# Performance work log

Hardware: AMD Instinct MI355X
Metric: run time of the kernel (lower is better)

## Reference

```python
import jax, jax.numpy as jnp
import numpy as np

B = 65536
MOTION, HIDDEN, LATENT, OUT = 256, 256, 64, 256
E, GH = 6, 64
INPUT = LATENT + MOTION   # 320, decoder layer-0 input width
INTER = LATENT + HIDDEN   # 320, decoder layers 1-3 input width


def _elu(x):
    return jax.nn.elu(x)


def _ln(x, s, b):
    m = jnp.mean(x, -1, keepdims=True)
    v = jnp.mean((x - m) ** 2, -1, keepdims=True)
    return (x - m) / jnp.sqrt(v + 1e-5) * s + b


def setup_inputs() -> dict:
    key = jax.random.key(0)
    ks = iter(jax.random.split(key, 64))

    def nrm(shape, scale=0.05):
        return jax.random.normal(next(ks), shape, jnp.float32) * scale

    d1 = [INPUT, INTER, INTER, INTER]   # per-layer expert weight in-dims
    d2 = [HIDDEN, HIDDEN, HIDDEN, OUT]  # per-layer expert weight out-dims
    inp = {
        'curr_state': jax.random.normal(next(ks), (B, MOTION), jnp.float32),
        'next_state': jax.random.normal(next(ks), (B, MOTION), jnp.float32),
        'eps': jax.random.normal(next(ks), (B, LATENT), jnp.float32),
        # encoder (torch Linear stored as [in, out])
        'enc_w1': nrm((2 * MOTION, HIDDEN)), 'enc_b1': nrm((HIDDEN,)),
        'enc_w2': nrm((HIDDEN, HIDDEN)), 'enc_b2': nrm((HIDDEN,)),
        'mu_w': nrm((HIDDEN, LATENT)), 'mu_b': nrm((LATENT,)),
        'lv_w': nrm((HIDDEN, LATENT)), 'lv_b': nrm((LATENT,)),
        # gating MLP
        'g_w1': nrm((INPUT, GH)), 'g_b1': nrm((GH,)),
        'g_w2': nrm((GH, GH)), 'g_b2': nrm((GH,)),
        'g_w3': nrm((GH, E)), 'g_b3': nrm((E,)),
    }
    for i in range(4):
        stdv = 1.0 / np.sqrt(d1[i])
        inp[f'w{i}'] = jax.random.uniform(next(ks), (E, d1[i], d2[i]), jnp.float32, -stdv, stdv)
        inp[f'b{i}'] = jax.random.uniform(next(ks), (E, d2[i]), jnp.float32, -stdv, stdv)
        inp[f'ln{i}_s'] = jnp.ones((d1[i],), jnp.float32)
        inp[f'ln{i}_b'] = jnp.zeros((d1[i],), jnp.float32)
    return inp


def reference(curr_state, next_state, eps,
              enc_w1, enc_b1, enc_w2, enc_b2, mu_w, mu_b, lv_w, lv_b,
              g_w1, g_b1, g_w2, g_b2, g_w3, g_b3,
              w0, b0, ln0_s, ln0_b, w1, b1, ln1_s, ln1_b,
              w2, b2, ln2_s, ln2_b, w3, b3, ln3_s, ln3_b):
    # ---- encoder ----
    h = _elu(jnp.concatenate([curr_state, next_state], -1) @ enc_w1 + enc_b1)
    h = _elu(h @ enc_w2 + enc_b2)
    mu = h @ mu_w + mu_b
    logvar = h @ lv_w + lv_b
    z = mu + eps * jnp.exp(0.5 * logvar)
    # ---- decoder(mu, curr_state): softmax-gated expert-weight blending ----
    x0 = jnp.concatenate([mu, curr_state], -1)            # [B, INPUT]
    g = _elu(x0 @ g_w1 + g_b1)
    g = _elu(g @ g_w2 + g_b2)
    coef = jax.nn.softmax(g @ g_w3 + g_b3, axis=-1)       # [B, E]
    ws, bs = (w0, w1, w2, w3), (b0, b1, b2, b3)
    lns = ((ln0_s, ln0_b), (ln1_s, ln1_b), (ln2_s, ln2_b), (ln3_s, ln3_b))
    out = None
    for i in range(4):
        xin = x0 if i == 0 else jnp.concatenate([mu, out], -1)
        xin = _ln(xin, *lns[i])
        mix = jnp.einsum('be,bj,ejk->bk', coef, xin, ws[i]) + coef @ bs[i]
        if i == 0:
            out = _elu(mix)
        elif i < 3:
            out = _elu(out + mix)
        else:
            out = mix
    return (out, z, mu, logvar)
```

## Files before the change

kernel.cpp:

```cpp
#include <hip/hip_runtime.h>
#include <hip/hip_bf16.h>
#include <stdint.h>


#define NB 65536
#define CHUNK 8192

typedef __attribute__((ext_vector_type(8))) short bf16x8;
typedef __attribute__((ext_vector_type(4))) float f32x4;

union FragU { bf16x8 v; unsigned int w[4]; uint4 u4; };

#define WP_E1   0
#define WP_E2   262144
#define WP_MULV 393216
#define WP_G1   458752
#define WP_G2   499712
#define WP_G3   507904
#define WP_DEC  509952
#define WP_BDEC 4442112
#define WP_COEF 4466688

#define L_XN     0
#define L_SCR    81920
#define L_WB     98304
#define LDS_ENC  147456
#define L_MUF   (L_XN + 2*CHUNK)
#define L_LVF   L_WB
#define L_HG1   L_WB
#define L_HG2   (L_WB + 32768)
#define L_G2W   L_SCR
#define L_G3W   (L_SCR + 8192)
#define L_SCORE (L_SCR + 10240)

#define B_XN     0
#define B_RAWMU  81920
#define B_COEF   98304
#define B_STATS  101376
#define B_PART   102400
#define B_PARTMU 106496
#define B_MUSTAT 110592
#define LDS_DEC  111616

__device__ __forceinline__ unsigned int pack2(float a, float b){
    __hip_bfloat162 h = __float22bfloat162_rn(make_float2(a, b));
    union { __hip_bfloat162 h2; unsigned int u; } cv; cv.h2 = h; return cv.u;
}
__device__ __forceinline__ unsigned short f2bf(float a){
    __hip_bfloat16 h = __float2bfloat16(a);
    union { __hip_bfloat16 h1; unsigned short u; } cv; cv.h1 = h; return cv.u;
}
__device__ __forceinline__ float eluf(float x){ return x > 0.f ? x : expm1f(x); }
__device__ __forceinline__ f32x4 mfma16(bf16x8 a, bf16x8 b, f32x4 c){
    return __builtin_amdgcn_mfma_f32_16x16x32_bf16(a, b, c, 0, 0, 0);
}
__device__ __forceinline__ void gload16(const void* g, void* l){
    __builtin_amdgcn_global_load_lds(
        (__attribute__((address_space(1))) unsigned int*)(uintptr_t)g,
        (__attribute__((address_space(3))) unsigned int*)(unsigned int)(uintptr_t)l,
        16, 0, 0);
}

template<int N> __device__ __forceinline__ void pipeV(){
    __builtin_amdgcn_sched_barrier(0);
    asm volatile("s_waitcnt vmcnt(%0)" :: "n"(N) : "memory");
    asm volatile("s_barrier" ::: "memory");
    __builtin_amdgcn_sched_barrier(0);
}
template<int N> __device__ __forceinline__ void pipeVL(){
    __builtin_amdgcn_sched_barrier(0);
    asm volatile("s_waitcnt vmcnt(%0) lgkmcnt(0)" :: "n"(N) : "memory");
    asm volatile("s_barrier" ::: "memory");
    __builtin_amdgcn_sched_barrier(0);
}
__device__ __forceinline__ void pipeL(){
    __builtin_amdgcn_sched_barrier(0);
    asm volatile("s_waitcnt lgkmcnt(0)" ::: "memory");
    asm volatile("s_barrier" ::: "memory");
    __builtin_amdgcn_sched_barrier(0);
}

__global__ void pack_small(const float* __restrict__ e1w, const float* __restrict__ e2w,
                           const float* __restrict__ muw, const float* __restrict__ lvw,
                           const float* __restrict__ g1w, const float* __restrict__ g2w,
                           const float* __restrict__ g3w, unsigned short* __restrict__ wsh){
    int p = blockIdx.x*256 + threadIdx.x;
    int local, k, n;
    auto decode = [&](int base, int NN){
        local = p - base;
        int i = local & 7, ln = (local>>3)&63, rest = local>>9;
        int ntg = rest % (NN/16), kb = rest / (NN/16);
        k = kb*32 + (ln>>4)*8 + i; n = ntg*16 + (ln&15);
    };
    if (p < 131072)      { decode(0,      256); wsh[WP_E1/2   + local] = f2bf(e1w[k*256+n]); }
    else if (p < 196608) { decode(131072, 256); wsh[WP_E2/2   + local] = f2bf(e2w[k*256+n]); }
    else if (p < 229376) { decode(196608, 128); wsh[WP_MULV/2 + local] = f2bf(n < 64 ? muw[k*64+n] : lvw[k*64+n-64]); }
    else if (p < 249856) { decode(229376,  64); wsh[WP_G1/2   + local] = f2bf(g1w[k*64+n]); }
    else if (p < 253952) { decode(249856,  64); wsh[WP_G2/2   + local] = f2bf(g2w[k*64+n]); }
    else                 { decode(253952,  16); wsh[WP_G3/2   + local] = f2bf(n < 6 ? g3w[k*6+n] : 0.f); }
}

__global__ void pack_dec(const float* __restrict__ w0, const float* __restrict__ w1,
                         const float* __restrict__ w2, const float* __restrict__ w3,
                         const float* __restrict__ s0, const float* __restrict__ s1,
                         const float* __restrict__ s2, const float* __restrict__ s3,
                         unsigned short* __restrict__ wsh){
    int p = blockIdx.x*256 + threadIdx.x;
    int i = p & 7, ln = (p>>3)&63, rest = p>>9;
    int ntg = rest & 15, r2 = rest >> 4;
    int kb = r2 % 10, r3 = r2 / 10;
    int e = r3 % 6, L = r3 / 6;
    int k = kb*32 + (ln>>4)*8 + i;
    int n = ntg*16 + (ln&15);
    const float* w = (L==0)?w0:(L==1)?w1:(L==2)?w2:w3;
    const float* s = (L==0)?s0:(L==1)?s1:(L==2)?s2:s3;
    wsh[WP_DEC/2 + p] = f2bf(s[k] * w[(e*320+k)*256 + n]);
}

__global__ void pack_bdec(const float* __restrict__ w0, const float* __restrict__ w1,
                          const float* __restrict__ w2, const float* __restrict__ w3,
                          const float* __restrict__ b0, const float* __restrict__ b1,
                          const float* __restrict__ b2, const float* __restrict__ b3,
                          const float* __restrict__ t0, const float* __restrict__ t1,
                          const float* __restrict__ t2, const float* __restrict__ t3,
                          float* __restrict__ outp){
    int t = blockIdx.x*256 + threadIdx.x;
    int n = t & 255, r = t >> 8;
    int e = r % 6, L = r / 6;
    const float* w  = (L==0)?w0:(L==1)?w1:(L==2)?w2:w3;
    const float* b  = (L==0)?b0:(L==1)?b1:(L==2)?b2:b3;
    const float* lb = (L==0)?t0:(L==1)?t1:(L==2)?t2:t3;
    float acc = b[e*256 + n];
    for (int k = 0; k < 320; ++k) acc += lb[k] * w[(e*320+k)*256 + n];
    outp[(L*6+e)*256 + n] = acc;
}

__global__ __launch_bounds__(512, 2) void vae_enc(
    const float* __restrict__ curr, const float* __restrict__ nxt,
    const float* __restrict__ eps,
    const float* __restrict__ eb1, const float* __restrict__ eb2,
    const float* __restrict__ mub, const float* __restrict__ lvb,
    const float* __restrict__ gb1, const float* __restrict__ gb2,
    const float* __restrict__ gb3,
    const unsigned short* __restrict__ wsh,
    float* __restrict__ coefws, float* __restrict__ dout)
{
    __shared__ __align__(16) char sm[LDS_ENC];
    const int tid  = threadIdx.x;
    const int lane = tid & 63;
    const int wave = tid >> 6;
    const int wr   = wave >> 2;
    const int wc   = wave & 3;
    const int l15  = lane & 15;
    const int lh   = lane >> 4;
    const long row0 = (long)blockIdx.x * 128;
    const char* wsb = (const char*)wsh;
    const f32x4 Z4 = {0.f, 0.f, 0.f, 0.f};

    const int aswz = ((lh ^ ((l15 >> 1) & 3)) << 4);
    int aoff[4];
    #pragma unroll
    for (int mt = 0; mt < 4; ++mt)
        aoff[mt] = ((((wr << 6) + (mt << 4) + l15)) << 6) + aswz;

    auto WB = [&](int i) -> int { return L_WB + i*16384; };
    auto stage16 = [&](long gOff, int ldsBase){
        gload16(wsb + gOff + ((long)wave << 10) + (lane << 4), sm + ldsBase + (wave << 10));
        gload16(wsb + gOff + ((long)(wave + 8) << 10) + (lane << 4), sm + ldsBase + ((wave + 8) << 10));
    };
    auto stage8 = [&](long gOff, int ldsBase){
        gload16(wsb + gOff + ((long)wave << 10) + (lane << 4), sm + ldsBase + (wave << 10));
    };
    auto stage4 = [&](long gOff, int ldsBase){
        int u = wave & 3;
        gload16(wsb + gOff + ((long)u << 10) + (lane << 4), sm + ldsBase + (u << 10));
    };
    auto loadB = [&](int bufBase, int idx) -> bf16x8 {
        FragU f; f.u4 = *(const uint4*)(sm + bufBase + (idx << 10) + (lane << 4));
        return f.v;
    };
    auto putRow = [&](int base, int n, int mt, const f32x4& v){
        char* cb = sm + base + ((n >> 5) * CHUNK);
        int col = n & 31;
        #pragma unroll
        for (int j = 0; j < 4; ++j){
            int r = (wr << 6) + (mt << 4) + (lh << 2) + j;
            *(unsigned short*)(cb + (r << 6) + ((((col >> 3) ^ ((r >> 1) & 3))) << 4)
                               + ((col & 7) << 1)) = f2bf(v[j]);
        }
    };

    f32x4 acc4[4][4];
    #pragma unroll
    for (int a = 0; a < 4; ++a)
        #pragma unroll
        for (int b = 0; b < 4; ++b) acc4[a][b] = Z4;
    {
        const int xrow = tid >> 2, xg = tid & 3;
        float4 xa, xb;
        auto loadX = [&](int kb){
            const float* src = (kb < 8) ? curr : nxt;
            const float* p = src + (row0 + xrow)*256 + (kb & 7)*32 + xg*8;
            xa = *(const float4*)p; xb = *(const float4*)(p + 4);
        };
        auto packX = [&](int slot){
            uint4 pk;
            pk.x = pack2(xa.x, xa.y); pk.y = pack2(xa.z, xa.w);
            pk.z = pack2(xb.x, xb.y); pk.w = pack2(xb.z, xb.w);
            *(uint4*)(sm + L_XN + slot*CHUNK + (xrow << 6)
                      + ((xg ^ ((xrow >> 1) & 3)) << 4)) = pk;
        };
        stage16(WP_E1, WB(0)); stage16(WP_E1 + 16384, WB(1));
        loadX(0); packX(0);
        loadX(1);
        #pragma unroll 1
        for (int s = 0; s < 16; ++s){
            pipeVL<4>();
            if (s + 2 < 16) stage16(WP_E1 + (long)(s + 2)*16384, WB((s + 2) % 3));
            if (s + 1 < 16){
                packX((s + 1) & 1);
                if (s + 2 < 16) loadX(s + 2);
            }
            int xbuf = L_XN + (s & 1)*CHUNK;
            int wb = WB(s % 3);
            FragU a[4];
            #pragma unroll
            for (int mt = 0; mt < 4; ++mt) a[mt].u4 = *(const uint4*)(sm + xbuf + aoff[mt]);
            #pragma unroll
            for (int nt = 0; nt < 4; ++nt){
                bf16x8 b = loadB(wb, wc*4 + nt);
                #pragma unroll
                for (int mt = 0; mt < 4; ++mt) acc4[mt][nt] = mfma16(a[mt].v, b, acc4[mt][nt]);
            }
        }
        pipeL();
        #pragma unroll
        for (int nt = 0; nt < 4; ++nt){
            int n = wc*64 + nt*16 + l15;
            float bias = eb1[n];
            #pragma unroll
            for (int mt = 0; mt < 4; ++mt){
                f32x4 v;
                #pragma unroll
                for (int j = 0; j < 4; ++j) v[j] = eluf(acc4[mt][nt][j] + bias);
                putRow(L_XN, n, mt, v);
            }
        }
        stage16(WP_E2, WB(0)); stage16(WP_E2 + 16384, WB(1));
        pipeL();
    }
    #pragma unroll
    for (int a = 0; a < 4; ++a)
        #pragma unroll
        for (int b = 0; b < 4; ++b) acc4[a][b] = Z4;
    {
        #pragma unroll 1
        for (int s = 0; s < 8; ++s){
            if (s + 1 < 8) pipeV<2>(); else pipeV<0>();
            if (s + 2 < 8) stage16(WP_E2 + (long)(s + 2)*16384, WB((s + 2) % 3));
            int wb = WB(s % 3);
            FragU a[4];
            #pragma unroll
            for (int mt = 0; mt < 4; ++mt)
                a[mt].u4 = *(const uint4*)(sm + L_XN + s*CHUNK + aoff[mt]);
            #pragma unroll
            for (int nt = 0; nt < 4; ++nt){
                bf16x8 b = loadB(wb, wc*4 + nt);
                #pragma unroll
                for (int mt = 0; mt < 4; ++mt) acc4[mt][nt] = mfma16(a[mt].v, b, acc4[mt][nt]);
            }
        }
        pipeL();
        #pragma unroll
        for (int nt = 0; nt < 4; ++nt){
            int n = wc*64 + nt*16 + l15;
            float bias = eb2[n];
            #pragma unroll
            for (int mt = 0; mt < 4; ++mt){
                f32x4 v;
                #pragma unroll
                for (int j = 0; j < 4; ++j) v[j] = eluf(acc4[mt][nt][j] + bias);
                putRow(L_XN, n, mt, v);
            }
        }
        stage8(WP_MULV, WB(0)); stage8(WP_MULV + 8192, WB(1));
        pipeL();
    }
    {
        f32x4 am[4][2];
        #pragma unroll
        for (int a = 0; a < 4; ++a){ am[a][0] = Z4; am[a][1] = Z4; }
        #pragma unroll 1
        for (int s = 0; s < 8; ++s){
            if (s + 1 < 8) pipeV<1>(); else pipeV<0>();
            if (s + 2 < 8) stage8(WP_MULV + (long)(s + 2)*8192, WB((s + 2) % 3));
            int wb = WB(s % 3);
            FragU a[4];
            #pragma unroll
            for (int mt = 0; mt < 4; ++mt)
                a[mt].u4 = *(const uint4*)(sm + L_XN + s*CHUNK + aoff[mt]);
            #pragma unroll
            for (int nt = 0; nt < 2; ++nt){
                bf16x8 b = loadB(wb, wc*2 + nt);
                #pragma unroll
                for (int mt = 0; mt < 4; ++mt) am[mt][nt] = mfma16(a[mt].v, b, am[mt][nt]);
            }
        }
        pipeL();
        #pragma unroll
        for (int nt = 0; nt < 2; ++nt){
            int n = wc*32 + nt*16 + l15;
            if (n < 64){
                float bias = mub[n];
                #pragma unroll
                for (int mt = 0; mt < 4; ++mt)
                    #pragma unroll
                    for (int j = 0; j < 4; ++j){
                        int r = (wr << 6) + (mt << 4) + (lh << 2) + j;
                        float v = am[mt][nt][j] + bias;
                        *(float*)(sm + L_MUF + (r << 8) + (n << 2)) = v;
                        dout[(long)NB*320 + (row0 + r)*64 + n] = v;
                    }
            } else {
                float bias = lvb[n - 64];
                #pragma unroll
                for (int mt = 0; mt < 4; ++mt)
                    #pragma unroll
                    for (int j = 0; j < 4; ++j){
                        int r = (wr << 6) + (mt << 4) + (lh << 2) + j;
                        float v = am[mt][nt][j] + bias;
                        *(float*)(sm + L_LVF + (r << 8) + ((n - 64) << 2)) = v;
                        dout[(long)NB*384 + (row0 + r)*64 + (n - 64)] = v;
                    }
            }
        }
        pipeL();
    }
    {
        int row = tid >> 2, seg = (tid & 3) << 4;
        float zm[16], zl[16];
        #pragma unroll
        for (int q = 0; q < 4; ++q){
            float4 m4 = *(const float4*)(sm + L_MUF + (row << 8) + ((seg + q*4) << 2));
            float4 l4 = *(const float4*)(sm + L_LVF + (row << 8) + ((seg + q*4) << 2));
            zm[q*4+0]=m4.x; zm[q*4+1]=m4.y; zm[q*4+2]=m4.z; zm[q*4+3]=m4.w;
            zl[q*4+0]=l4.x; zl[q*4+1]=l4.y; zl[q*4+2]=l4.z; zl[q*4+3]=l4.w;
        }
        const float* ep = eps + (row0 + row)*64 + seg;
        float* zo = dout + (long)NB*256 + (row0 + row)*64 + seg;
        #pragma unroll
        for (int q = 0; q < 4; ++q){
            float4 e4 = *(const float4*)(ep + q*4);
            float4 z4;
            z4.x = zm[q*4+0] + e4.x * expf(0.5f*zl[q*4+0]);
            z4.y = zm[q*4+1] + e4.y * expf(0.5f*zl[q*4+1]);
            z4.z = zm[q*4+2] + e4.z * expf(0.5f*zl[q*4+2]);
            z4.w = zm[q*4+3] + e4.w * expf(0.5f*zl[q*4+3]);
            *(float4*)(zo + q*4) = z4;
        }
        uint4 pkA, pkB;
        pkA.x = pack2(zm[0],  zm[1]);  pkA.y = pack2(zm[2],  zm[3]);
        pkA.z = pack2(zm[4],  zm[5]);  pkA.w = pack2(zm[6],  zm[7]);
        pkB.x = pack2(zm[8],  zm[9]);  pkB.y = pack2(zm[10], zm[11]);
        pkB.z = pack2(zm[12], zm[13]); pkB.w = pack2(zm[14], zm[15]);
        int c = seg >> 5, g0 = (seg & 31) >> 3, sw = (row >> 1) & 3;
        char* cb = sm + L_XN + c*CHUNK + (row << 6);
        *(uint4*)(cb + ((g0 ^ sw) << 4))       = pkA;
        *(uint4*)(cb + (((g0 + 1) ^ sw) << 4)) = pkB;
    }
    pipeL();
    #pragma unroll
    for (int c = 0; c < 2; ++c){
        int idx = c*512 + tid;
        int row = idx & 127, kbi = idx >> 7;
        const float* p = curr + (row0 + row)*256 + kbi*32;
        char* cb = sm + L_XN + (2 + kbi)*CHUNK + (row << 6);
        int sw = (row >> 1) & 3;
        #pragma unroll
        for (int g = 0; g < 4; ++g){
            float4 fa = *(const float4*)(p + g*8);
            float4 fb = *(const float4*)(p + g*8 + 4);
            uint4 pk;
            pk.x = pack2(fa.x, fa.y); pk.y = pack2(fa.z, fa.w);
            pk.z = pack2(fb.x, fb.y); pk.w = pack2(fb.z, fb.w);
            *(uint4*)(cb + ((g ^ sw) << 4)) = pk;
        }
    }
    stage4(WP_G1, WB(0)); stage4(WP_G1 + 4096, WB(1));
    pipeL();
    {
        f32x4 ga[4];
        #pragma unroll
        for (int a = 0; a < 4; ++a) ga[a] = Z4;
        #pragma unroll 1
        for (int s = 0; s < 10; ++s){
            if (s + 1 < 10) pipeV<1>(); else pipeV<0>();
            if (s + 2 < 10) stage4(WP_G1 + (long)(s + 2)*4096, WB((s + 2) % 3));
            int wb = WB(s % 3);
            bf16x8 b = loadB(wb, wc);
            #pragma unroll
            for (int mt = 0; mt < 4; ++mt){
                FragU a; a.u4 = *(const uint4*)(sm + L_XN + s*CHUNK + aoff[mt]);
                ga[mt] = mfma16(a.v, b, ga[mt]);
            }
        }
        pipeL();
        {
            int n = wc*16 + l15;
            float bias = gb1[n];
            #pragma unroll
            for (int mt = 0; mt < 4; ++mt){
                f32x4 v;
                #pragma unroll
                for (int j = 0; j < 4; ++j) v[j] = eluf(ga[mt][j] + bias);
                putRow(L_HG1, n, mt, v);
            }
        }
        stage8(WP_G2, L_G2W);
        if (wave < 2)
            gload16(wsb + WP_G3 + ((long)wave << 10) + (lane << 4),
                    sm + L_G3W + (wave << 10));
        pipeVL<0>();
        #pragma unroll
        for (int a = 0; a < 4; ++a) ga[a] = Z4;
        #pragma unroll
        for (int kb = 0; kb < 2; ++kb){
            bf16x8 b = loadB(L_G2W, kb*4 + wc);
            #pragma unroll
            for (int mt = 0; mt < 4; ++mt){
                FragU a; a.u4 = *(const uint4*)(sm + L_HG1 + kb*CHUNK + aoff[mt]);
                ga[mt] = mfma16(a.v, b, ga[mt]);
            }
        }
        pipeL();
        {
            int n = wc*16 + l15;
            float bias = gb2[n];
            #pragma unroll
            for (int mt = 0; mt < 4; ++mt){
                f32x4 v;
                #pragma unroll
                for (int j = 0; j < 4; ++j) v[j] = eluf(ga[mt][j] + bias);
                putRow(L_HG2, n, mt, v);
            }
        }
        pipeL();
        if (wc == 0){
            f32x4 sc[4];
            #pragma unroll
            for (int a = 0; a < 4; ++a) sc[a] = Z4;
            #pragma unroll
            for (int kb = 0; kb < 2; ++kb){
                bf16x8 b = loadB(L_G3W, kb);
                #pragma unroll
                for (int mt = 0; mt < 4; ++mt){
                    FragU a; a.u4 = *(const uint4*)(sm + L_HG2 + kb*CHUNK + aoff[mt]);
                    sc[mt] = mfma16(a.v, b, sc[mt]);
                }
            }
            if (l15 < 8){
                float bias = (l15 < 6) ? gb3[l15] : 0.f;
                #pragma unroll
                for (int mt = 0; mt < 4; ++mt)
                    #pragma unroll
                    for (int j = 0; j < 4; ++j){
                        int r = (wr << 6) + (mt << 4) + (lh << 2) + j;
                        *(float*)(sm + L_SCORE + (r << 5) + (l15 << 2)) = sc[mt][j] + bias;
                    }
            }
        }
        pipeL();
        if (tid < 128){
            float s[6];
            #pragma unroll
            for (int e = 0; e < 6; ++e) s[e] = *(const float*)(sm + L_SCORE + (tid << 5) + (e << 2));
            float m = s[0];
            #pragma unroll
            for (int e = 1; e < 6; ++e) m = fmaxf(m, s[e]);
            float sum = 0.f;
            #pragma unroll
            for (int e = 0; e < 6; ++e){ s[e] = expf(s[e] - m); sum += s[e]; }
            float inv = 1.f / sum;
            float* cw = coefws + (long)blockIdx.x * 768;
            #pragma unroll
            for (int e = 0; e < 6; ++e) cw[e*128 + tid] = s[e] * inv;
        }
    }
}

__global__ __launch_bounds__(512, 2) void vae_dec(
    const float* __restrict__ curr,
    const unsigned short* __restrict__ wsh, const float* __restrict__ bdec,
    const float* __restrict__ coefws, float* __restrict__ dout)
{
    __shared__ __align__(16) char sm[LDS_DEC];
    const int tid  = threadIdx.x;
    const int lane = tid & 63;
    const int wave = tid >> 6;
    const int wr   = wave >> 2;
    const int wc   = wave & 3;
    const int l15  = lane & 15;
    const int lh   = lane >> 4;
    const long row0 = (long)blockIdx.x * 128;
    const char* wsb = (const char*)wsh;
    const f32x4 Z4 = {0.f, 0.f, 0.f, 0.f};

    const int aswz = ((lh ^ ((l15 >> 1) & 3)) << 4);
    int aoff[4];
    #pragma unroll
    for (int mt = 0; mt < 4; ++mt)
        aoff[mt] = ((((wr << 6) + (mt << 4) + l15)) << 6) + aswz;

    auto putRow = [&](int base, int n, int mt, const f32x4& v){
        char* cb = sm + base + ((n >> 5) * CHUNK);
        int col = n & 31;
        #pragma unroll
        for (int j = 0; j < 4; ++j){
            int r = (wr << 6) + (mt << 4) + (lh << 2) + j;
            *(unsigned short*)(cb + (r << 6) + ((((col >> 3) ^ ((r >> 1) & 3))) << 4)
                               + ((col & 7) << 1)) = f2bf(v[j]);
        }
    };

    #pragma unroll
    for (int rep = 0; rep < 2; ++rep){
        int i = rep*512 + tid;
        if (i < 768) *(float*)(sm + B_COEF + (i << 2)) = coefws[(long)blockIdx.x*768 + i];
    }
    {
        int row = tid >> 2, seg = (tid & 3) << 4;
        const float* mp = dout + (long)NB*320 + (row0 + row)*64 + seg;
        float zm[16];
        #pragma unroll
        for (int q = 0; q < 4; ++q){
            float4 m4 = *(const float4*)(mp + q*4);
            zm[q*4+0]=m4.x; zm[q*4+1]=m4.y; zm[q*4+2]=m4.z; zm[q*4+3]=m4.w;
        }
        uint4 pkA, pkB;
        pkA.x = pack2(zm[0],  zm[1]);  pkA.y = pack2(zm[2],  zm[3]);
        pkA.z = pack2(zm[4],  zm[5]);  pkA.w = pack2(zm[6],  zm[7]);
        pkB.x = pack2(zm[8],  zm[9]);  pkB.y = pack2(zm[10], zm[11]);
        pkB.z = pack2(zm[12], zm[13]); pkB.w = pack2(zm[14], zm[15]);
        int c = seg >> 5, g0 = (seg & 31) >> 3, sw = (row >> 1) & 3;
        char* cb = sm + B_XN + c*CHUNK + (row << 6);
        *(uint4*)(cb + ((g0 ^ sw) << 4))       = pkA;
        *(uint4*)(cb + (((g0 + 1) ^ sw) << 4)) = pkB;
    }
    #pragma unroll
    for (int c = 0; c < 2; ++c){
        int idx = c*512 + tid;
        int row = idx & 127, kbi = idx >> 7;
        const float* p = curr + (row0 + row)*256 + kbi*32;
        char* cb = sm + B_XN + (2 + kbi)*CHUNK + (row << 6);
        int sw = (row >> 1) & 3;
        #pragma unroll
        for (int g = 0; g < 4; ++g){
            float4 fa = *(const float4*)(p + g*8);
            float4 fb = *(const float4*)(p + g*8 + 4);
            uint4 pk;
            pk.x = pack2(fa.x, fa.y); pk.y = pack2(fa.z, fa.w);
            pk.z = pack2(fb.x, fb.y); pk.w = pack2(fb.z, fb.w);
            *(uint4*)(cb + ((g ^ sw) << 4)) = pk;
        }
    }
    __syncthreads();
    {
        int row = tid >> 2, part = tid & 3;
        int go = ((part ^ ((row >> 1) & 3)) << 4);
        float s = 0.f, q = 0.f, smu = 0.f, qmu = 0.f;
        #pragma unroll
        for (int c = 0; c < 10; ++c){
            uint4 d = *(const uint4*)(sm + B_XN + c*CHUNK + (row << 6) + go);
            const unsigned int* dw = (const unsigned int*)&d;
            float ls = 0.f, lq = 0.f;
            #pragma unroll
            for (int u = 0; u < 4; ++u){
                float lo = __uint_as_float(dw[u] << 16);
                float hi = __uint_as_float(dw[u] & 0xffff0000u);
                ls += lo + hi; lq += lo*lo + hi*hi;
            }
            s += ls; q += lq;
            if (c < 2){ smu += ls; qmu += lq; }
        }
        *(float2*)(sm + B_PART   + (((row << 2) + part) << 3)) = make_float2(s, q);
        *(float2*)(sm + B_PARTMU + (((row << 2) + part) << 3)) = make_float2(smu, qmu);
    }
    __syncthreads();
    if (tid < 128){
        float S = 0.f, Q = 0.f, Sm = 0.f, Qm = 0.f;
        #pragma unroll
        for (int pp = 0; pp < 4; ++pp){
            float2 f = *(const float2*)(sm + B_PART   + (((tid << 2) + pp) << 3));
            float2 g = *(const float2*)(sm + B_PARTMU + (((tid << 2) + pp) << 3));
            S += f.x; Q += f.y; Sm += g.x; Qm += g.y;
        }
        float mean = S * (1.f/320.f);
        float var  = Q * (1.f/320.f) - mean*mean;
        *(float2*)(sm + B_STATS  + (tid << 3)) = make_float2(mean, rsqrtf(var + 1e-5f));
        *(float2*)(sm + B_MUSTAT + (tid << 3)) = make_float2(Sm, Qm);
    }
    __syncthreads();
    {
        int row = tid >> 2, part = tid & 3;
        int go = ((part ^ ((row >> 1) & 3)) << 4);
        float2 st = *(const float2*)(sm + B_STATS + (row << 3));
        #pragma unroll
        for (int c = 0; c < 10; ++c){
            char* p = sm + B_XN + c*CHUNK + (row << 6) + go;
            uint4 d = *(const uint4*)p;
            if (c < 2) *(uint4*)(sm + B_RAWMU + c*CHUNK + (row << 6) + go) = d;
            const unsigned int* dw = (const unsigned int*)&d;
            uint4 o; unsigned int* ow = (unsigned int*)&o;
            #pragma unroll
            for (int u = 0; u < 4; ++u){
                float lo = (__uint_as_float(dw[u] << 16)         - st.x) * st.y;
                float hi = (__uint_as_float(dw[u] & 0xffff0000u) - st.x) * st.y;
                ow[u] = pack2(lo, hi);
            }
            *(uint4*)p = o;
        }
    }
    __syncthreads();

    f32x4 master[4][4], acc[4][4];
    #pragma unroll
    for (int a = 0; a < 4; ++a)
        #pragma unroll
        for (int b = 0; b < 4; ++b) master[a][b] = Z4;

    #pragma unroll 1
    for (int L = 0; L < 4; ++L){
        const char* wLb = wsb + WP_DEC + (((long)L*60) << 14) + (lane << 4)
                          + ((wc*4) << 10);
        FragU bA[4], bB[4];
        auto loadBG = [&](FragU* bd, int s){
            const char* p = wLb + ((long)s << 14);
            #pragma unroll
            for (int nt = 0; nt < 4; ++nt)
                bd[nt].u4 = *(const uint4*)(p + (nt << 10));
        };
        auto doStep = [&](FragU* bd, int s){
            int e  = s / 10;
            int kb = s - e*10;
            FragU a[4];
            #pragma unroll
            for (int mt = 0; mt < 4; ++mt)
                a[mt].u4 = *(const uint4*)(sm + B_XN + kb*CHUNK + aoff[mt]);
            if (kb == 0){
                #pragma unroll
                for (int x = 0; x < 4; ++x)
                    #pragma unroll
                    for (int y = 0; y < 4; ++y) acc[x][y] = Z4;
            }
            #pragma unroll
            for (int nt = 0; nt < 4; ++nt)
                #pragma unroll
                for (int mt = 0; mt < 4; ++mt)
                    acc[mt][nt] = mfma16(a[mt].v, bd[nt].v, acc[mt][nt]);
            if (kb == 9){
                #pragma unroll
                for (int mt = 0; mt < 4; ++mt){
                    f32x4 cq = *(const f32x4*)(sm + B_COEF +
                                ((e*128 + (wr << 6) + (mt << 4) + (lh << 2)) << 2));
                    #pragma unroll
                    for (int nt = 0; nt < 4; ++nt)
                        #pragma unroll
                        for (int j = 0; j < 4; ++j)
                            master[mt][nt][j] = fmaf(cq[j], acc[mt][nt][j], master[mt][nt][j]);
                }
            }
        };
        loadBG(bA, 0);
        #pragma unroll 1
        for (int s = 0; s < 60; s += 2){
            loadBG(bB, s + 1);
            doStep(bA, s);
            if (s + 2 < 60) loadBG(bA, s + 2);
            doStep(bB, s + 1);
        }
        __syncthreads();

        {
            float bv[6][4];
            #pragma unroll
            for (int ee = 0; ee < 6; ++ee)
                #pragma unroll
                for (int nt = 0; nt < 4; ++nt)
                    bv[ee][nt] = bdec[((L*6 + ee) << 8) + wc*64 + nt*16 + l15];
            #pragma unroll
            for (int mt = 0; mt < 4; ++mt){
                f32x4 cq[6];
                #pragma unroll
                for (int ee = 0; ee < 6; ++ee)
                    cq[ee] = *(const f32x4*)(sm + B_COEF +
                              ((ee*128 + (wr << 6) + (mt << 4) + (lh << 2)) << 2));
                #pragma unroll
                for (int nt = 0; nt < 4; ++nt){
                    int n = wc*64 + nt*16 + l15;
                    f32x4 v;
                    #pragma unroll
                    for (int j = 0; j < 4; ++j){
                        float bias = cq[0][j]*bv[0][nt] + cq[1][j]*bv[1][nt]
                                   + cq[2][j]*bv[2][nt] + cq[3][j]*bv[3][nt]
                                   + cq[4][j]*bv[4][nt] + cq[5][j]*bv[5][nt];
                        float mix = master[mt][nt][j] + bias;
                        v[j] = (L == 3) ? mix : eluf(mix);
                    }
                    if (L < 3){
                        acc[mt][nt] = v;
                        master[mt][nt] = (L < 2) ? v : Z4;
                    } else {
                        #pragma unroll
                        for (int j = 0; j < 4; ++j){
                            int r = (wr << 6) + (mt << 4) + (lh << 2) + j;
                            dout[(row0 + r)*256 + n] = v[j];
                        }
                    }
                }
            }
        }
        if (L < 3){
            #pragma unroll
            for (int mt = 0; mt < 4; ++mt){
                f32x4 sv = acc[mt][0] + acc[mt][1] + acc[mt][2] + acc[mt][3];
                f32x4 qv = acc[mt][0]*acc[mt][0] + acc[mt][1]*acc[mt][1]
                         + acc[mt][2]*acc[mt][2] + acc[mt][3]*acc[mt][3];
                #pragma unroll
                for (int x = 1; x < 16; x <<= 1){
                    #pragma unroll
                    for (int j = 0; j < 4; ++j){
                        sv[j] += __shfl_xor(sv[j], x);
                        qv[j] += __shfl_xor(qv[j], x);
                    }
                }
                if (l15 == 0){
                    #pragma unroll
                    for (int j = 0; j < 4; ++j){
                        int r = (wr << 6) + (mt << 4) + (lh << 2) + j;
                        *(float2*)(sm + B_PART + (((r << 2) + wc) << 3)) = make_float2(sv[j], qv[j]);
                    }
                }
            }
            __syncthreads();
            if (tid < 128){
                float2 mu2 = *(const float2*)(sm + B_MUSTAT + (tid << 3));
                float S = mu2.x, Q = mu2.y;
                #pragma unroll
                for (int pp = 0; pp < 4; ++pp){
                    float2 f = *(const float2*)(sm + B_PART + (((tid << 2) + pp) << 3));
                    S += f.x; Q += f.y;
                }
                float mean = S * (1.f/320.f);
                float var  = Q * (1.f/320.f) - mean*mean;
                *(float2*)(sm + B_STATS + (tid << 3)) = make_float2(mean, rsqrtf(var + 1e-5f));
            }
            __syncthreads();
            #pragma unroll
            for (int mt = 0; mt < 4; ++mt){
                int r0 = (wr << 6) + (mt << 4) + (lh << 2);
                float4 p0 = *(const float4*)(sm + B_STATS + (r0 << 3));
                float4 p1 = *(const float4*)(sm + B_STATS + (r0 << 3) + 16);
                float mj[4] = {p0.x, p0.z, p1.x, p1.z};
                float rj[4] = {p0.y, p0.w, p1.y, p1.w};
                #pragma unroll
                for (int nt = 0; nt < 4; ++nt){
                    int n = wc*64 + nt*16 + l15;
                    f32x4 xn;
                    #pragma unroll
                    for (int j = 0; j < 4; ++j) xn[j] = (acc[mt][nt][j] - mj[j]) * rj[j];
                    putRow(B_XN + 2*CHUNK, n, mt, xn);
                }
            }
            #pragma unroll
            for (int rep = 0; rep < 2; ++rep){
                int gi = rep*512 + tid;
                int c = gi >> 9, row = (gi >> 2) & 127, g2 = gi & 3;
                float2 st = *(const float2*)(sm + B_STATS + (row << 3));
                uint4 d = *(const uint4*)(sm + B_RAWMU + c*CHUNK + (row << 6) + (g2 << 4));
                const unsigned int* dw = (const unsigned int*)&d;
                uint4 o; unsigned int* ow = (unsigned int*)&o;
                #pragma unroll
                for (int u = 0; u < 4; ++u){
                    float lo = (__uint_as_float(dw[u] << 16)         - st.x) * st.y;
                    float hi = (__uint_as_float(dw[u] & 0xffff0000u) - st.x) * st.y;
                    ow[u] = pack2(lo, hi);
                }
                *(uint4*)(sm + B_XN + c*CHUNK + (row << 6) + (g2 << 4)) = o;
            }
            __syncthreads();
        }
    }
}

extern "C" void kernel_launch(void* const* d_in, const int* in_sizes, int n_in,
                              void* d_out, int out_size, void* d_ws, size_t ws_size,
                              hipStream_t stream)
{
    (void)in_sizes; (void)n_in; (void)out_size; (void)ws_size;
    const float* curr = (const float*)d_in[0];
    const float* nxt  = (const float*)d_in[1];
    const float* eps  = (const float*)d_in[2];
    const float* ew1  = (const float*)d_in[3];
    const float* eb1  = (const float*)d_in[4];
    const float* ew2  = (const float*)d_in[5];
    const float* eb2  = (const float*)d_in[6];
    const float* muw  = (const float*)d_in[7];
    const float* mub  = (const float*)d_in[8];
    const float* lvw  = (const float*)d_in[9];
    const float* lvb  = (const float*)d_in[10];
    const float* gw1  = (const float*)d_in[11];
    const float* gb1  = (const float*)d_in[12];
    const float* gw2  = (const float*)d_in[13];
    const float* gb2  = (const float*)d_in[14];
    const float* gw3  = (const float*)d_in[15];
    const float* gb3  = (const float*)d_in[16];
    const float* w0 = (const float*)d_in[17]; const float* b0 = (const float*)d_in[18];
    const float* s0 = (const float*)d_in[19]; const float* t0 = (const float*)d_in[20];
    const float* w1 = (const float*)d_in[21]; const float* b1 = (const float*)d_in[22];
    const float* s1 = (const float*)d_in[23]; const float* t1 = (const float*)d_in[24];
    const float* w2 = (const float*)d_in[25]; const float* b2 = (const float*)d_in[26];
    const float* s2 = (const float*)d_in[27]; const float* t2 = (const float*)d_in[28];
    const float* w3 = (const float*)d_in[29]; const float* b3 = (const float*)d_in[30];
    const float* s3 = (const float*)d_in[31]; const float* t3 = (const float*)d_in[32];

    unsigned short* wsh = (unsigned short*)d_ws;
    float* bdec   = (float*)((char*)d_ws + WP_BDEC);
    float* coefws = (float*)((char*)d_ws + WP_COEF);
    float* dout   = (float*)d_out;

    hipLaunchKernelGGL(pack_small, dim3(996), dim3(256), 0, stream,
                       ew1, ew2, muw, lvw, gw1, gw2, gw3, wsh);
    hipLaunchKernelGGL(pack_dec, dim3(7680), dim3(256), 0, stream,
                       w0, w1, w2, w3, s0, s1, s2, s3, wsh);
    hipLaunchKernelGGL(pack_bdec, dim3(24), dim3(256), 0, stream,
                       w0, w1, w2, w3, b0, b1, b2, b3, t0, t1, t2, t3, bdec);
    hipLaunchKernelGGL(vae_enc, dim3(512), dim3(512), 0, stream,
                       curr, nxt, eps, eb1, eb2, mub, lvb, gb1, gb2, gb3,
                       wsh, coefws, dout);
    hipLaunchKernelGGL(vae_dec, dim3(512), dim3(512), 0, stream,
                       curr, wsh, bdec, coefws, dout);
}
```

Measured before the change: 530.6 us.

## Halve decoder block rows to 64 for higher occupancy and smaller LDS

The decoder kernel now processes 64 rows per block instead of 128. All 8 waves share those rows and each wave takes a 32-column slice of the output. The raw-mu LDS copy is dropped and mu is re-read from global memory at each layer, which shrinks LDS to about 51KB and allows launch bounds of 4 blocks per CU with twice as many blocks. In exchange, each block reads the same B weight fragments for half as many rows, doubling weight traffic from L2, and there are extra global reloads of mu.

Result: faster. 496.5 us (-6.4%).

```diff
diff --git a/kernel.cpp b/kernel.cpp
--- a/kernel.cpp
+++ b/kernel.cpp
@@ -5,6 +5,7 @@
 
 #define NB 65536
 #define CHUNK 8192
+#define CH64  4096
 
 typedef __attribute__((ext_vector_type(8))) short bf16x8;
 typedef __attribute__((ext_vector_type(4))) float f32x4;
@@ -33,14 +34,13 @@
 #define L_G3W   (L_SCR + 8192)
 #define L_SCORE (L_SCR + 10240)
 
-#define B_XN     0
-#define B_RAWMU  81920
-#define B_COEF   98304
-#define B_STATS  101376
-#define B_PART   102400
-#define B_PARTMU 106496
-#define B_MUSTAT 110592
-#define LDS_DEC  111616
+#define D_XN     0
+#define D_COEF   40960
+#define D_STATS  42496
+#define D_PART   43008
+#define D_PARTMU 47104
+#define D_MUSTAT 51200
+#define LDS_DEC  51712
 
 __device__ __forceinline__ unsigned int pack2(float a, float b){
     __hip_bfloat162 h = __float22bfloat162_rn(make_float2(a, b));
@@ -488,7 +488,7 @@
     }
 }
 
-__global__ __launch_bounds__(512, 2) void vae_dec(
+__global__ __launch_bounds__(512, 4) void vae_dec(
     const float* __restrict__ curr,
     const unsigned short* __restrict__ wsh, const float* __restrict__ bdec,
     const float* __restrict__ coefws, float* __restrict__ dout)
@@ -496,12 +496,11 @@
     __shared__ __align__(16) char sm[LDS_DEC];
     const int tid  = threadIdx.x;
     const int lane = tid & 63;
-    const int wave = tid >> 6;
-    const int wr   = wave >> 2;
-    const int wc   = wave & 3;
+    const int w    = tid >> 6;
     const int l15  = lane & 15;
     const int lh   = lane >> 4;
-    const long row0 = (long)blockIdx.x * 128;
+    const long row0 = (long)blockIdx.x * 64;
+    const int eb   = blockIdx.x >> 1, half = blockIdx.x & 1;
     const char* wsb = (const char*)wsh;
     const f32x4 Z4 = {0.f, 0.f, 0.f, 0.f};
 
@@ -509,49 +508,37 @@
     int aoff[4];
     #pragma unroll
     for (int mt = 0; mt < 4; ++mt)
-        aoff[mt] = ((((wr << 6) + (mt << 4) + l15)) << 6) + aswz;
+        aoff[mt] = (((mt << 4) + l15) << 6) + aswz;
 
     auto putRow = [&](int base, int n, int mt, const f32x4& v){
-        char* cb = sm + base + ((n >> 5) * CHUNK);
+        char* cb = sm + base + ((n >> 5) * CH64);
         int col = n & 31;
         #pragma unroll
         for (int j = 0; j < 4; ++j){
-            int r = (wr << 6) + (mt << 4) + (lh << 2) + j;
+            int r = (mt << 4) + (lh << 2) + j;
             *(unsigned short*)(cb + (r << 6) + ((((col >> 3) ^ ((r >> 1) & 3))) << 4)
                                + ((col & 7) << 1)) = f2bf(v[j]);
         }
     };
 
-    #pragma unroll
-    for (int rep = 0; rep < 2; ++rep){
-        int i = rep*512 + tid;
-        if (i < 768) *(float*)(sm + B_COEF + (i << 2)) = coefws[(long)blockIdx.x*768 + i];
-    }
+    if (tid < 384)
+        *(float*)(sm + D_COEF + (tid << 2)) =
+            coefws[(long)eb*768 + (tid >> 6)*128 + half*64 + (tid & 63)];
     {
-        int row = tid >> 2, seg = (tid & 3) << 4;
+        int row = tid >> 3, seg = (tid & 7) << 3;
         const float* mp = dout + (long)NB*320 + (row0 + row)*64 + seg;
-        float zm[16];
-        #pragma unroll
-        for (int q = 0; q < 4; ++q){
-            float4 m4 = *(const float4*)(mp + q*4);
-            zm[q*4+0]=m4.x; zm[q*4+1]=m4.y; zm[q*4+2]=m4.z; zm[q*4+3]=m4.w;
-        }
-        uint4 pkA, pkB;
-        pkA.x = pack2(zm[0],  zm[1]);  pkA.y = pack2(zm[2],  zm[3]);
-        pkA.z = pack2(zm[4],  zm[5]);  pkA.w = pack2(zm[6],  zm[7]);
-        pkB.x = pack2(zm[8],  zm[9]);  pkB.y = pack2(zm[10], zm[11]);
-        pkB.z = pack2(zm[12], zm[13]); pkB.w = pack2(zm[14], zm[15]);
-        int c = seg >> 5, g0 = (seg & 31) >> 3, sw = (row >> 1) & 3;
-        char* cb = sm + B_XN + c*CHUNK + (row << 6);
-        *(uint4*)(cb + ((g0 ^ sw) << 4))       = pkA;
-        *(uint4*)(cb + (((g0 + 1) ^ sw) << 4)) = pkB;
-    }
-    #pragma unroll
-    for (int c = 0; c < 2; ++c){
-        int idx = c*512 + tid;
-        int row = idx & 127, kbi = idx >> 7;
+        float4 a4 = *(const float4*)mp;
+        float4 b4 = *(const float4*)(mp + 4);
+        uint4 pk;
+        pk.x = pack2(a4.x, a4.y); pk.y = pack2(a4.z, a4.w);
+        pk.z = pack2(b4.x, b4.y); pk.w = pack2(b4.z, b4.w);
+        int g0 = seg >> 3, c = g0 >> 2, gg = g0 & 3, sw = (row >> 1) & 3;
+        *(uint4*)(sm + D_XN + c*CH64 + (row << 6) + ((gg ^ sw) << 4)) = pk;
+    }
+    {
+        int row = tid & 63, kbi = tid >> 6;
         const float* p = curr + (row0 + row)*256 + kbi*32;
-        char* cb = sm + B_XN + (2 + kbi)*CHUNK + (row << 6);
+        char* cb = sm + D_XN + (2 + kbi)*CH64 + (row << 6);
         int sw = (row >> 1) & 3;
         #pragma unroll
         for (int g = 0; g < 4; ++g){
@@ -565,12 +552,14 @@
     }
     __syncthreads();
     {
-        int row = tid >> 2, part = tid & 3;
-        int go = ((part ^ ((row >> 1) & 3)) << 4);
+        int row = tid >> 3, part = tid & 7;
+        int sw = (row >> 1) & 3;
         float s = 0.f, q = 0.f, smu = 0.f, qmu = 0.f;
         #pragma unroll
-        for (int c = 0; c < 10; ++c){
-            uint4 d = *(const uint4*)(sm + B_XN + c*CHUNK + (row << 6) + go);
+        for (int k = 0; k < 5; ++k){
+            int g = part + (k << 3);
+            int c = g >> 2, gg = g & 3;
+            uint4 d = *(const uint4*)(sm + D_XN + c*CH64 + (row << 6) + ((gg ^ sw) << 4));
             const unsigned int* dw = (const unsigned int*)&d;
             float ls = 0.f, lq = 0.f;
             #pragma unroll
@@ -580,35 +569,36 @@
                 ls += lo + hi; lq += lo*lo + hi*hi;
             }
             s += ls; q += lq;
-            if (c < 2){ smu += ls; qmu += lq; }
-        }
-        *(float2*)(sm + B_PART   + (((row << 2) + part) << 3)) = make_float2(s, q);
-        *(float2*)(sm + B_PARTMU + (((row << 2) + part) << 3)) = make_float2(smu, qmu);
+            if (k == 0){ smu = ls; qmu = lq; }
+        }
+        *(float2*)(sm + D_PART   + (((row << 3) + part) << 3)) = make_float2(s, q);
+        *(float2*)(sm + D_PARTMU + (((row << 3) + part) << 3)) = make_float2(smu, qmu);
     }
     __syncthreads();
-    if (tid < 128){
+    if (tid < 64){
         float S = 0.f, Q = 0.f, Sm = 0.f, Qm = 0.f;
         #pragma unroll
-        for (int pp = 0; pp < 4; ++pp){
-            float2 f = *(const float2*)(sm + B_PART   + (((tid << 2) + pp) << 3));
-            float2 g = *(const float2*)(sm + B_PARTMU + (((tid << 2) + pp) << 3));
+        for (int pp = 0; pp < 8; ++pp){
+            float2 f = *(const float2*)(sm + D_PART   + (((tid << 3) + pp) << 3));
+            float2 g = *(const float2*)(sm + D_PARTMU + (((tid << 3) + pp) << 3));
             S += f.x; Q += f.y; Sm += g.x; Qm += g.y;
         }
         float mean = S * (1.f/320.f);
         float var  = Q * (1.f/320.f) - mean*mean;
-        *(float2*)(sm + B_STATS  + (tid << 3)) = make_float2(mean, rsqrtf(var + 1e-5f));
-        *(float2*)(sm + B_MUSTAT + (tid << 3)) = make_float2(Sm, Qm);
+        *(float2*)(sm + D_STATS  + (tid << 3)) = make_float2(mean, rsqrtf(var + 1e-5f));
+        *(float2*)(sm + D_MUSTAT + (tid << 3)) = make_float2(Sm, Qm);
     }
     __syncthreads();
     {
-        int row = tid >> 2, part = tid & 3;
-        int go = ((part ^ ((row >> 1) & 3)) << 4);
-        float2 st = *(const float2*)(sm + B_STATS + (row << 3));
-        #pragma unroll
-        for (int c = 0; c < 10; ++c){
-            char* p = sm + B_XN + c*CHUNK + (row << 6) + go;
+        int row = tid >> 3, part = tid & 7;
+        int sw = (row >> 1) & 3;
+        float2 st = *(const float2*)(sm + D_STATS + (row << 3));
+        #pragma unroll
+        for (int k = 0; k < 5; ++k){
+            int g = part + (k << 3);
+            int c = g >> 2, gg = g & 3;
+            char* p = sm + D_XN + c*CH64 + (row << 6) + ((gg ^ sw) << 4);
             uint4 d = *(const uint4*)p;
-            if (c < 2) *(uint4*)(sm + B_RAWMU + c*CHUNK + (row << 6) + go) = d;
             const unsigned int* dw = (const unsigned int*)&d;
             uint4 o; unsigned int* ow = (unsigned int*)&o;
             #pragma unroll
@@ -622,22 +612,19 @@
     }
     __syncthreads();
 
-    f32x4 master[4][4], acc[4][4];
+    f32x4 master[4][2], acc[4][2];
     #pragma unroll
-    for (int a = 0; a < 4; ++a)
-        #pragma unroll
-        for (int b = 0; b < 4; ++b) master[a][b] = Z4;
+    for (int a = 0; a < 4; ++a){ master[a][0] = Z4; master[a][1] = Z4; }
 
     #pragma unroll 1
     for (int L = 0; L < 4; ++L){
         const char* wLb = wsb + WP_DEC + (((long)L*60) << 14) + (lane << 4)
-                          + ((wc*4) << 10);
-        FragU bA[4], bB[4];
+                          + ((w*2) << 10);
+        FragU bA[2], bB[2];
         auto loadBG = [&](FragU* bd, int s){
             const char* p = wLb + ((long)s << 14);
-            #pragma unroll
-            for (int nt = 0; nt < 4; ++nt)
-                bd[nt].u4 = *(const uint4*)(p + (nt << 10));
+            bd[0].u4 = *(const uint4*)p;
+            bd[1].u4 = *(const uint4*)(p + 1024);
         };
         auto doStep = [&](FragU* bd, int s){
             int e  = s / 10;
@@ -645,25 +632,23 @@
             FragU a[4];
             #pragma unroll
             for (int mt = 0; mt < 4; ++mt)
-                a[mt].u4 = *(const uint4*)(sm + B_XN + kb*CHUNK + aoff[mt]);
+                a[mt].u4 = *(const uint4*)(sm + D_XN + kb*CH64 + aoff[mt]);
             if (kb == 0){
                 #pragma unroll
-                for (int x = 0; x < 4; ++x)
-                    #pragma unroll
-                    for (int y = 0; y < 4; ++y) acc[x][y] = Z4;
-            }
-            #pragma unroll
-            for (int nt = 0; nt < 4; ++nt)
+                for (int x = 0; x < 4; ++x){ acc[x][0] = Z4; acc[x][1] = Z4; }
+            }
+            #pragma unroll
+            for (int nt = 0; nt < 2; ++nt)
                 #pragma unroll
                 for (int mt = 0; mt < 4; ++mt)
                     acc[mt][nt] = mfma16(a[mt].v, bd[nt].v, acc[mt][nt]);
             if (kb == 9){
                 #pragma unroll
                 for (int mt = 0; mt < 4; ++mt){
-                    f32x4 cq = *(const f32x4*)(sm + B_COEF +
-                                ((e*128 + (wr << 6) + (mt << 4) + (lh << 2)) << 2));
+                    f32x4 cq = *(const f32x4*)(sm + D_COEF +
+                                ((e*64 + (mt << 4) + (lh << 2)) << 2));
                     #pragma unroll
-                    for (int nt = 0; nt < 4; ++nt)
+                    for (int nt = 0; nt < 2; ++nt)
                         #pragma unroll
                         for (int j = 0; j < 4; ++j)
                             master[mt][nt][j] = fmaf(cq[j], acc[mt][nt][j], master[mt][nt][j]);
@@ -681,22 +666,22 @@
         __syncthreads();
 
         {
-            float bv[6][4];
+            float bv[6][2];
             #pragma unroll
             for (int ee = 0; ee < 6; ++ee)
                 #pragma unroll
-                for (int nt = 0; nt < 4; ++nt)
-                    bv[ee][nt] = bdec[((L*6 + ee) << 8) + wc*64 + nt*16 + l15];
+                for (int nt = 0; nt < 2; ++nt)
+                    bv[ee][nt] = bdec[((L*6 + ee) << 8) + w*32 + nt*16 + l15];
             #pragma unroll
             for (int mt = 0; mt < 4; ++mt){
                 f32x4 cq[6];
                 #pragma unroll
                 for (int ee = 0; ee < 6; ++ee)
-                    cq[ee] = *(const f32x4*)(sm + B_COEF +
-                              ((ee*128 + (wr << 6) + (mt << 4) + (lh << 2)) << 2));
-                #pragma unroll
-                for (int nt = 0; nt < 4; ++nt){
-                    int n = wc*64 + nt*16 + l15;
+                    cq[ee] = *(const f32x4*)(sm + D_COEF +
+                              ((ee*64 + (mt << 4) + (lh << 2)) << 2));
+                #pragma unroll
+                for (int nt = 0; nt < 2; ++nt){
+                    int n = w*32 + nt*16 + l15;
                     f32x4 v;
                     #pragma unroll
                     for (int j = 0; j < 4; ++j){
@@ -712,7 +697,7 @@
                     } else {
                         #pragma unroll
                         for (int j = 0; j < 4; ++j){
-                            int r = (wr << 6) + (mt << 4) + (lh << 2) + j;
+                            int r = (mt << 4) + (lh << 2) + j;
                             dout[(row0 + r)*256 + n] = v[j];
                         }
                     }
@@ -722,9 +707,8 @@
         if (L < 3){
             #pragma unroll
             for (int mt = 0; mt < 4; ++mt){
-                f32x4 sv = acc[mt][0] + acc[mt][1] + acc[mt][2] + acc[mt][3];
-                f32x4 qv = acc[mt][0]*acc[mt][0] + acc[mt][1]*acc[mt][1]
-                         + acc[mt][2]*acc[mt][2] + acc[mt][3]*acc[mt][3];
+                f32x4 sv = acc[mt][0] + acc[mt][1];
+                f32x4 qv = acc[mt][0]*acc[mt][0] + acc[mt][1]*acc[mt][1];
                 #pragma unroll
                 for (int x = 1; x < 16; x <<= 1){
                     #pragma unroll
@@ -736,56 +720,54 @@
                 if (l15 == 0){
                     #pragma unroll
                     for (int j = 0; j < 4; ++j){
-                        int r = (wr << 6) + (mt << 4) + (lh << 2) + j;
-                        *(float2*)(sm + B_PART + (((r << 2) + wc) << 3)) = make_float2(sv[j], qv[j]);
+                        int r = (mt << 4) + (lh << 2) + j;
+                        *(float2*)(sm + D_PART + (((r << 3) + w) << 3)) = make_float2(sv[j], qv[j]);
                     }
                 }
             }
             __syncthreads();
-            if (tid < 128){
-                float2 mu2 = *(const float2*)(sm + B_MUSTAT + (tid << 3));
+            if (tid < 64){
+                float2 mu2 = *(const float2*)(sm + D_MUSTAT + (tid << 3));
                 float S = mu2.x, Q = mu2.y;
                 #pragma unroll
-                for (int pp = 0; pp < 4; ++pp){
-                    float2 f = *(const float2*)(sm + B_PART + (((tid << 2) + pp) << 3));
+                for (int pp = 0; pp < 8; ++pp){
+                    float2 f = *(const float2*)(sm + D_PART + (((tid << 3) + pp) << 3));
                     S += f.x; Q += f.y;
                 }
                 float mean = S * (1.f/320.f);
                 float var  = Q * (1.f/320.f) - mean*mean;
-                *(float2*)(sm + B_STATS + (tid << 3)) = make_float2(mean, rsqrtf(var + 1e-5f));
+                *(float2*)(sm + D_STATS + (tid << 3)) = make_float2(mean, rsqrtf(var + 1e-5f));
             }
             __syncthreads();
             #pragma unroll
             for (int mt = 0; mt < 4; ++mt){
-                int r0 = (wr << 6) + (mt << 4) + (lh << 2);
-                float4 p0 = *(const float4*)(sm + B_STATS + (r0 << 3));
-                float4 p1 = *(const float4*)(sm + B_STATS + (r0 << 3) + 16);
+                int r0 = (mt << 4) + (lh << 2);
+                float4 p0 = *(const float4*)(sm + D_STATS + (r0 << 3));
+                float4 p1 = *(const float4*)(sm + D_STATS + (r0 << 3) + 16);
                 float mj[4] = {p0.x, p0.z, p1.x, p1.z};
                 float rj[4] = {p0.y, p0.w, p1.y, p1.w};
                 #pragma unroll
-                for (int nt = 0; nt < 4; ++nt){
-                    int n = wc*64 + nt*16 + l15;
+                for (int nt = 0; nt < 2; ++nt){
+                    int n = w*32 + nt*16 + l15;
                     f32x4 xn;
                     #pragma unroll
                     for (int j = 0; j < 4; ++j) xn[j] = (acc[mt][nt][j] - mj[j]) * rj[j];
-                    putRow(B_XN + 2*CHUNK, n, mt, xn);
+                    putRow(D_XN + 2*CH64, n, mt, xn);
                 }
             }
-            #pragma unroll
-            for (int rep = 0; rep < 2; ++rep){
-                int gi = rep*512 + tid;
-                int c = gi >> 9, row = (gi >> 2) & 127, g2 = gi & 3;
-                float2 st = *(const float2*)(sm + B_STATS + (row << 3));
-                uint4 d = *(const uint4*)(sm + B_RAWMU + c*CHUNK + (row << 6) + (g2 << 4));
-                const unsigned int* dw = (const unsigned int*)&d;
-                uint4 o; unsigned int* ow = (unsigned int*)&o;
-                #pragma unroll
-                for (int u = 0; u < 4; ++u){
-                    float lo = (__uint_as_float(dw[u] << 16)         - st.x) * st.y;
-                    float hi = (__uint_as_float(dw[u] & 0xffff0000u) - st.x) * st.y;
-                    ow[u] = pack2(lo, hi);
-                }
-                *(uint4*)(sm + B_XN + c*CHUNK + (row << 6) + (g2 << 4)) = o;
+            {
+                int row = tid >> 3, seg = (tid & 7) << 3;
+                const float* mp = dout + (long)NB*320 + (row0 + row)*64 + seg;
+                float4 a4 = *(const float4*)mp;
+                float4 b4 = *(const float4*)(mp + 4);
+                float2 st = *(const float2*)(sm + D_STATS + (row << 3));
+                uint4 pk;
+                pk.x = pack2((a4.x - st.x)*st.y, (a4.y - st.x)*st.y);
+                pk.y = pack2((a4.z - st.x)*st.y, (a4.w - st.x)*st.y);
+                pk.z = pack2((b4.x - st.x)*st.y, (b4.y - st.x)*st.y);
+                pk.w = pack2((b4.z - st.x)*st.y, (b4.w - st.x)*st.y);
+                int g0 = seg >> 3, c = g0 >> 2, gg = g0 & 3, sw = (row >> 1) & 3;
+                *(uint4*)(sm + D_XN + c*CH64 + (row << 6) + ((gg ^ sw) << 4)) = pk;
             }
             __syncthreads();
         }
@@ -837,6 +819,6 @@
     hipLaunchKernelGGL(vae_enc, dim3(512), dim3(512), 0, stream,
                        curr, nxt, eps, eb1, eb2, mub, lvb, gb1, gb2, gb3,
                        wsh, coefws, dout);
-    hipLaunchKernelGGL(vae_dec, dim3(512), dim3(512), 0, stream,
+    hipLaunchKernelGGL(vae_dec, dim3(1024), dim3(512), 0, stream,
                        curr, wsh, bdec, coefws, dout);
 }
```
